# Optimization experiments

Hardware: AMD Instinct MI355X
Metric: run time of the kernel (lower is better)

Reference implementation:

```python
import jax, jax.numpy as jnp
import numpy as np

B = 8192          # batch
DIM = 2048        # feature dim
FANOUT = 10       # balanced 10-ary tree, depth 3 -> 1000 leaves
N_NODES = 1 + 10 + 100  # inner nodes with classifiers = 111
NUM_CLASSES = 1000


def setup_inputs() -> dict:
    key = jax.random.key(0)
    k1, k2, k3, k4 = jax.random.split(key, 4)
    x = jax.random.normal(k1, (B, DIM), dtype=jnp.float32)
    labels = jax.random.randint(k2, (B,), 0, NUM_CLASSES, dtype=jnp.int64 if jax.config.jax_enable_x64 else jnp.int32)
    # Stacked per-node Linear(dim, num_child+1): column 0 is the extra slot
    # included in the softmax but never routed to (children use cols 1..FANOUT).
    W = jax.random.normal(k3, (N_NODES, DIM, FANOUT + 1), dtype=jnp.float32) * (1.0 / np.sqrt(DIM))
    b = jax.random.normal(k4, (N_NODES, FANOUT + 1), dtype=jnp.float32) * 0.01
    return {"x": x, "labels": labels, "W": W, "b": b}


def reference(x, labels, W, b):
    # All 111 tiny per-node Linear+softmax classifiers fused into one batched GEMM.
    logits = jnp.einsum('bd,ndk->bnk', x, W) + b          # [B, 111, 11]
    probs = jax.nn.softmax(logits, axis=-1)               # softmax over num_child+1 (incl. dummy col 0)
    # Hierarchical path probabilities (root.path_prob = 1.0):
    # level-1 nodes are children of root (node 0), via softmax columns 1..10.
    p1 = probs[:, 0, 1:]                                   # [B, 10]
    # level-2 nodes: children of nodes 1..10
    p2 = (p1[:, :, None] * probs[:, 1:11, 1:]).reshape(x.shape[0], 100)    # [B, 100]
    # leaves: children of nodes 11..110 -> 1000 classes (out[:, 1:] slice already applied)
    out = (p2[:, :, None] * probs[:, 11:111, 1:]).reshape(x.shape[0], NUM_CLASSES)  # [B, 1000]
    penalty = jnp.float32(0.0)
    return (out, penalty)
```

## Files before the change

### kernel.cpp

```cpp
#include <hip/hip_runtime.h>
#include <hip/hip_bf16.h>
#include <hip/hip_fp16.h>

typedef _Float16 f16;
typedef __attribute__((ext_vector_type(8))) _Float16 f16x8;
typedef __attribute__((ext_vector_type(4))) float f32x4;

#define DIM     2048
#define BROWS   8192
#define NCOLS   1221
#define NPAD    1280
#define NNODES  111
#define BK      64
#define NKT     (DIM / BK)
#define IMG     8192
#define PANEL   (32 * IMG)

__global__ __launch_bounds__(256) void prep_x(const float* __restrict__ X,
                                              f16* __restrict__ Xf) {
    __shared__ float T[128 * 68];
    int blk = blockIdx.x;
    int mp = blk >> 5, kt = blk & 31;
    int t = threadIdx.x;
    int row = t >> 1, half = t & 1;
    const float* src = X + (size_t)(mp * 128 + row) * DIM + kt * 64 + half * 32;
    float* dst = T + row * 68 + half * 32;
    #pragma unroll
    for (int i = 0; i < 8; ++i) ((f32x4*)dst)[i] = ((const f32x4*)src)[i];
    __syncthreads();
    int w = t >> 6, l = t & 63, r = l & 15, q = l >> 4;
    f16* out = Xf + (size_t)blk * IMG;
    #pragma unroll
    for (int p = 0; p < 4; ++p) {
        int gk = p * 4 + w;
        int kk = gk >> 3, g = gk & 7;
        const float* s = T + (g * 16 + r) * 68 + kk * 32 + q * 8;
        f32x4 a = *(const f32x4*)s;
        f32x4 b = *(const f32x4*)(s + 4);
        f16x8 h;
        h[0] = (f16)a[0]; h[1] = (f16)a[1]; h[2] = (f16)a[2]; h[3] = (f16)a[3];
        h[4] = (f16)b[0]; h[5] = (f16)b[1]; h[6] = (f16)b[2]; h[7] = (f16)b[3];
        *(f16x8*)(out + (size_t)(p * 256 + t) * 8) = h;
    }
}

__global__ void prep_b(const float* __restrict__ W, f16* __restrict__ Bf) {
    int idx = blockIdx.x * 256 + threadIdx.x;
    int c = idx & 1023, img = idx >> 10;
    int np = img >> 5, kt = img & 31;
    int kk = c >> 9, g = (c >> 6) & 7, l = c & 63, r = l & 15, q = l >> 4;
    int col = np * 128 + g * 16 + r;
    int d0  = kt * 64 + kk * 32 + q * 8;
    f16x8 v;
    if (col < NCOLS) {
        int n = col / 11, k = col - n * 11;
        const float* src = W + ((size_t)n * DIM + d0) * 11 + k;
        #pragma unroll
        for (int e = 0; e < 8; ++e) v[e] = (f16)src[(size_t)e * 11];
    } else {
        #pragma unroll
        for (int e = 0; e < 8; ++e) v[e] = (f16)0.f;
    }
    *(f16x8*)(Bf + (size_t)idx * 8) = v;
}

__global__ __launch_bounds__(512, 2) void gemm_f16(const f16* __restrict__ Xf,
                                                   const f16* __restrict__ Bf,
                                                   f16* __restrict__ Lh) {
    __shared__ __align__(16) f16 As[2][16384];
    __shared__ __align__(16) f16 Bs[2][16384];

    int bid = blockIdx.x;
    int swz = (bid & 7) * 20 + (bid >> 3);
    int mt = swz / 5, nt = swz - mt * 5;

    int t = threadIdx.x, w = t >> 6, l = t & 63, r = l & 15, q = l >> 4;
    int wm = w >> 2, wn = w & 3;

    const f16* abase = Xf + (size_t)(mt * 2) * PANEL + (size_t)t * 8;
    const f16* bbase = Bf + (size_t)(nt * 2) * PANEL + (size_t)t * 8;

    f32x4 acc[8][4];
    #pragma unroll
    for (int i = 0; i < 8; ++i)
        #pragma unroll
        for (int j = 0; j < 4; ++j) acc[i][j] = (f32x4)0.f;

#define STAGE(KT, C)                                                              \
    {                                                                             \
        _Pragma("unroll")                                                         \
        for (int p = 0; p < 4; ++p) {                                             \
            __builtin_amdgcn_global_load_lds(                                     \
                (const __attribute__((address_space(1))) void*)                   \
                    (abase + (size_t)(p >> 1) * PANEL + (size_t)(KT) * IMG + (p & 1) * 4096), \
                (__attribute__((address_space(3))) void*)(&As[C][p * 4096 + w * 512]), 16, 0, 0); \
            __builtin_amdgcn_global_load_lds(                                     \
                (const __attribute__((address_space(1))) void*)                   \
                    (bbase + (size_t)(p >> 1) * PANEL + (size_t)(KT) * IMG + (p & 1) * 4096), \
                (__attribute__((address_space(3))) void*)(&Bs[C][p * 4096 + w * 512]), 16, 0, 0); \
        }                                                                         \
    }

#define COMPUTE(C)                                                                \
    {                                                                             \
        _Pragma("unroll")                                                         \
        for (int kk = 0; kk < 2; ++kk) {                                          \
            f16x8 af[8], bfr[4];                                                  \
            _Pragma("unroll")                                                     \
            for (int m = 0; m < 8; ++m)                                           \
                af[m] = *(const f16x8*)(&As[C][wm * 8192 + ((kk * 8 + m) * 64 + l) * 8]); \
            _Pragma("unroll")                                                     \
            for (int n = 0; n < 4; ++n)                                           \
                bfr[n] = *(const f16x8*)(&Bs[C][(wn >> 1) * 8192                  \
                            + ((kk * 8 + (wn & 1) * 4 + n) * 64 + l) * 8]);       \
            _Pragma("unroll")                                                     \
            for (int m = 0; m < 8; ++m)                                           \
                _Pragma("unroll")                                                 \
                for (int n = 0; n < 4; ++n)                                       \
                    acc[m][n] = __builtin_amdgcn_mfma_f32_16x16x32_f16(af[m], bfr[n], acc[m][n], 0, 0, 0); \
        }                                                                         \
    }

    STAGE(0, 0)

    for (int kt = 0; kt < NKT - 1; ++kt) {
        int cc = kt & 1, cn = cc ^ 1;
        STAGE(kt + 1, cn)
        asm volatile("s_waitcnt vmcnt(8)" ::: "memory");
        __builtin_amdgcn_s_barrier();
        COMPUTE(cc)
        asm volatile("s_waitcnt lgkmcnt(0)" ::: "memory");
        __builtin_amdgcn_s_barrier();
    }
    asm volatile("s_waitcnt vmcnt(0)" ::: "memory");
    __builtin_amdgcn_s_barrier();
    COMPUTE(1)

#undef STAGE
#undef COMPUTE

    #pragma unroll
    for (int m = 0; m < 8; ++m) {
        int row = mt * 256 + wm * 128 + m * 16 + q * 4;
        #pragma unroll
        for (int n = 0; n < 4; ++n) {
            int col = nt * 256 + wn * 64 + n * 16 + r;
            #pragma unroll
            for (int j = 0; j < 4; ++j)
                Lh[(size_t)(row + j) * NPAD + col] = (f16)acc[m][n][j];
        }
    }
}

__global__ void tree_epi(const f16* __restrict__ L, const float* __restrict__ bias,
                         float* __restrict__ out) {
    __shared__ float P[4][NNODES * 11];
    __shared__ f16 R[4][NPAD];
    int w = threadIdx.x >> 6, l = threadIdx.x & 63;
    int row = blockIdx.x * 4 + w;

    const f16x8* src = (const f16x8*)(L + (size_t)row * NPAD);
    f16x8* dst = (f16x8*)R[w];
    dst[l]      = src[l];
    dst[l + 64] = src[l + 64];
    if (l < 32) dst[l + 128] = src[l + 128];

    for (int n = l; n < NNODES; n += 64) {
        float v[11], mx = -1e30f;
        #pragma unroll
        for (int k = 0; k < 11; ++k) { v[k] = (float)R[w][n * 11 + k] + bias[n * 11 + k]; mx = fmaxf(mx, v[k]); }
        float s = 0.f;
        #pragma unroll
        for (int k = 0; k < 11; ++k) { v[k] = __expf(v[k] - mx); s += v[k]; }
        float inv = 1.f / s;
        #pragma unroll
        for (int k = 0; k < 11; ++k) P[w][n * 11 + k] = v[k] * inv;
    }
    __syncthreads();
    const float* Pw = P[w];
    for (int c = l; c < 1000; c += 64) {
        int i  = c / 100;
        int j  = (c % 100) / 10;
        int mm = c % 10;
        float p = Pw[1 + i] * Pw[(1 + i) * 11 + 1 + j] * Pw[(11 + 10 * i + j) * 11 + 1 + mm];
        out[(size_t)row * 1000 + c] = p;
    }
    if (row == 0 && threadIdx.x == 0) out[(size_t)BROWS * 1000] = 0.f;
}

extern "C" void kernel_launch(void* const* d_in, const int* in_sizes, int n_in,
                              void* d_out, int out_size, void* d_ws, size_t ws_size,
                              hipStream_t stream) {
    const float* x    = (const float*)d_in[0];
    const float* W    = (const float*)d_in[2];
    const float* bias = (const float*)d_in[3];
    float* out = (float*)d_out;

    f16* Xf = (f16*)d_ws;
    f16* Bf = (f16*)((char*)d_ws + 33554432);
    f16* Lh = (f16*)((char*)d_ws + 38797312);

    prep_x <<<64 * 32, 256, 0, stream>>>(x, Xf);
    prep_b <<<1280, 256, 0, stream>>>(W, Bf);
    gemm_f16<<<160, 512, 0, stream>>>(Xf, Bf, Lh);
    tree_epi<<<BROWS / 4, 256, 0, stream>>>(Lh, bias, out);
}
```

Before: 104.2 us.

## Interleave split-K loads with MFMA phases and merge prep kernels into one launch

The GEMM main loop now stages each half-K slice of the A and B tiles separately and interleaves those global-to-LDS loads with four smaller MFMA phases. Each phase is separated by barriers and surrounded by wave priority raising, with finer vmcnt waits. This is meant to overlap memory traffic with matrix math more evenly, at the cost of more barriers per iteration. The two prep kernels are also fused into one launch that branches on block index, saving one launch and letting X conversion and W conversion run concurrently.

```diff
diff --git a/kernel.cpp b/kernel.cpp
--- a/kernel.cpp
+++ b/kernel.cpp
@@ -12,56 +12,58 @@
 #define NPAD    1280
 #define NNODES  111
 #define BK      64
-#define NKT     (DIM / BK)
+#define NKT     32
 #define IMG     8192
 #define PANEL   (32 * IMG)
 
-__global__ __launch_bounds__(256) void prep_x(const float* __restrict__ X,
-                                              f16* __restrict__ Xf) {
+__global__ __launch_bounds__(256) void prep_all(const float* __restrict__ X,
+                                                const float* __restrict__ W,
+                                                f16* __restrict__ Xf,
+                                                f16* __restrict__ Bf) {
     __shared__ float T[128 * 68];
-    int blk = blockIdx.x;
-    int mp = blk >> 5, kt = blk & 31;
-    int t = threadIdx.x;
-    int row = t >> 1, half = t & 1;
-    const float* src = X + (size_t)(mp * 128 + row) * DIM + kt * 64 + half * 32;
-    float* dst = T + row * 68 + half * 32;
-    #pragma unroll
-    for (int i = 0; i < 8; ++i) ((f32x4*)dst)[i] = ((const f32x4*)src)[i];
-    __syncthreads();
-    int w = t >> 6, l = t & 63, r = l & 15, q = l >> 4;
-    f16* out = Xf + (size_t)blk * IMG;
-    #pragma unroll
-    for (int p = 0; p < 4; ++p) {
-        int gk = p * 4 + w;
-        int kk = gk >> 3, g = gk & 7;
-        const float* s = T + (g * 16 + r) * 68 + kk * 32 + q * 8;
-        f32x4 a = *(const f32x4*)s;
-        f32x4 b = *(const f32x4*)(s + 4);
-        f16x8 h;
-        h[0] = (f16)a[0]; h[1] = (f16)a[1]; h[2] = (f16)a[2]; h[3] = (f16)a[3];
-        h[4] = (f16)b[0]; h[5] = (f16)b[1]; h[6] = (f16)b[2]; h[7] = (f16)b[3];
-        *(f16x8*)(out + (size_t)(p * 256 + t) * 8) = h;
-    }
-}
-
-__global__ void prep_b(const float* __restrict__ W, f16* __restrict__ Bf) {
-    int idx = blockIdx.x * 256 + threadIdx.x;
-    int c = idx & 1023, img = idx >> 10;
-    int np = img >> 5, kt = img & 31;
-    int kk = c >> 9, g = (c >> 6) & 7, l = c & 63, r = l & 15, q = l >> 4;
-    int col = np * 128 + g * 16 + r;
-    int d0  = kt * 64 + kk * 32 + q * 8;
-    f16x8 v;
-    if (col < NCOLS) {
-        int n = col / 11, k = col - n * 11;
-        const float* src = W + ((size_t)n * DIM + d0) * 11 + k;
-        #pragma unroll
-        for (int e = 0; e < 8; ++e) v[e] = (f16)src[(size_t)e * 11];
+    int b = blockIdx.x;
+    if (b < 2048) {
+        int mp = b >> 5, kt = b & 31;
+        int t = threadIdx.x;
+        int row = t >> 1, half = t & 1;
+        const float* src = X + (size_t)(mp * 128 + row) * DIM + kt * 64 + half * 32;
+        float* dst = T + row * 68 + half * 32;
+        #pragma unroll
+        for (int i = 0; i < 8; ++i) ((f32x4*)dst)[i] = ((const f32x4*)src)[i];
+        __syncthreads();
+        int w = t >> 6, l = t & 63, r = l & 15, q = l >> 4;
+        f16* out = Xf + (size_t)b * IMG;
+        #pragma unroll
+        for (int p = 0; p < 4; ++p) {
+            int gk = p * 4 + w;
+            int kk = gk >> 3, g = gk & 7;
+            const float* s = T + (g * 16 + r) * 68 + kk * 32 + q * 8;
+            f32x4 a = *(const f32x4*)s;
+            f32x4 c = *(const f32x4*)(s + 4);
+            f16x8 h;
+            h[0] = (f16)a[0]; h[1] = (f16)a[1]; h[2] = (f16)a[2]; h[3] = (f16)a[3];
+            h[4] = (f16)c[0]; h[5] = (f16)c[1]; h[6] = (f16)c[2]; h[7] = (f16)c[3];
+            *(f16x8*)(out + (size_t)(p * 256 + t) * 8) = h;
+        }
     } else {
-        #pragma unroll
-        for (int e = 0; e < 8; ++e) v[e] = (f16)0.f;
-    }
-    *(f16x8*)(Bf + (size_t)idx * 8) = v;
+        int idx = (b - 2048) * 256 + threadIdx.x;
+        int c = idx & 1023, img = idx >> 10;
+        int np = img >> 5, kt = img & 31;
+        int kk = c >> 9, g = (c >> 6) & 7, l = c & 63, r = l & 15, q = l >> 4;
+        int col = np * 128 + g * 16 + r;
+        int d0  = kt * 64 + kk * 32 + q * 8;
+        f16x8 v;
+        if (col < NCOLS) {
+            int n = col / 11, k = col - n * 11;
+            const float* src = W + ((size_t)n * DIM + d0) * 11 + k;
+            #pragma unroll
+            for (int e = 0; e < 8; ++e) v[e] = (f16)src[(size_t)e * 11];
+        } else {
+            #pragma unroll
+            for (int e = 0; e < 8; ++e) v[e] = (f16)0.f;
+        }
+        *(f16x8*)(Bf + (size_t)idx * 8) = v;
+    }
 }
 
 __global__ __launch_bounds__(512, 2) void gemm_f16(const f16* __restrict__ Xf,
@@ -76,6 +78,7 @@
 
     int t = threadIdx.x, w = t >> 6, l = t & 63, r = l & 15, q = l >> 4;
     int wm = w >> 2, wn = w & 3;
+    int bpan = (wn >> 1) * 8192, bc4 = (wn & 1) * 4;
 
     const f16* abase = Xf + (size_t)(mt * 2) * PANEL + (size_t)t * 8;
     const f16* bbase = Bf + (size_t)(nt * 2) * PANEL + (size_t)t * 8;
@@ -86,58 +89,94 @@
         #pragma unroll
         for (int j = 0; j < 4; ++j) acc[i][j] = (f32x4)0.f;
 
-#define STAGE(KT, C)                                                              \
-    {                                                                             \
-        _Pragma("unroll")                                                         \
-        for (int p = 0; p < 4; ++p) {                                             \
-            __builtin_amdgcn_global_load_lds(                                     \
-                (const __attribute__((address_space(1))) void*)                   \
-                    (abase + (size_t)(p >> 1) * PANEL + (size_t)(KT) * IMG + (p & 1) * 4096), \
-                (__attribute__((address_space(3))) void*)(&As[C][p * 4096 + w * 512]), 16, 0, 0); \
-            __builtin_amdgcn_global_load_lds(                                     \
-                (const __attribute__((address_space(1))) void*)                   \
-                    (bbase + (size_t)(p >> 1) * PANEL + (size_t)(KT) * IMG + (p & 1) * 4096), \
-                (__attribute__((address_space(3))) void*)(&Bs[C][p * 4096 + w * 512]), 16, 0, 0); \
-        }                                                                         \
-    }
-
-#define COMPUTE(C)                                                                \
-    {                                                                             \
-        _Pragma("unroll")                                                         \
-        for (int kk = 0; kk < 2; ++kk) {                                          \
-            f16x8 af[8], bfr[4];                                                  \
-            _Pragma("unroll")                                                     \
-            for (int m = 0; m < 8; ++m)                                           \
-                af[m] = *(const f16x8*)(&As[C][wm * 8192 + ((kk * 8 + m) * 64 + l) * 8]); \
-            _Pragma("unroll")                                                     \
-            for (int n = 0; n < 4; ++n)                                           \
-                bfr[n] = *(const f16x8*)(&Bs[C][(wn >> 1) * 8192                  \
-                            + ((kk * 8 + (wn & 1) * 4 + n) * 64 + l) * 8]);       \
-            _Pragma("unroll")                                                     \
-            for (int m = 0; m < 8; ++m)                                           \
-                _Pragma("unroll")                                                 \
-                for (int n = 0; n < 4; ++n)                                       \
-                    acc[m][n] = __builtin_amdgcn_mfma_f32_16x16x32_f16(af[m], bfr[n], acc[m][n], 0, 0, 0); \
-        }                                                                         \
-    }
-
-    STAGE(0, 0)
-
-    for (int kt = 0; kt < NKT - 1; ++kt) {
-        int cc = kt & 1, cn = cc ^ 1;
-        STAGE(kt + 1, cn)
-        asm volatile("s_waitcnt vmcnt(8)" ::: "memory");
-        __builtin_amdgcn_s_barrier();
-        COMPUTE(cc)
-        asm volatile("s_waitcnt lgkmcnt(0)" ::: "memory");
-        __builtin_amdgcn_s_barrier();
-    }
-    asm volatile("s_waitcnt vmcnt(0)" ::: "memory");
-    __builtin_amdgcn_s_barrier();
-    COMPUTE(1)
-
-#undef STAGE
-#undef COMPUTE
+    f16x8 af[4], bfr[4];
+
+#define GLD(SRC, DST)                                                            \
+    __builtin_amdgcn_global_load_lds(                                            \
+        (const __attribute__((address_space(1))) void*)(SRC),                    \
+        (__attribute__((address_space(3))) void*)(DST), 16, 0, 0)
+#define STAGE_A(KT, C, KH)                                                       \
+    { GLD(abase + (size_t)(KT) * IMG + (KH) * 4096, &As[C][(KH) * 4096 + w * 512]);            \
+      GLD(abase + PANEL + (size_t)(KT) * IMG + (KH) * 4096, &As[C][(2 + (KH)) * 4096 + w * 512]); }
+#define STAGE_B(KT, C, KH)                                                       \
+    { GLD(bbase + (size_t)(KT) * IMG + (KH) * 4096, &Bs[C][(KH) * 4096 + w * 512]);            \
+      GLD(bbase + PANEL + (size_t)(KT) * IMG + (KH) * 4096, &Bs[C][(2 + (KH)) * 4096 + w * 512]); }
+#define DS_AF(C, KK, MH)                                                         \
+    { _Pragma("unroll")                                                          \
+      for (int m_ = 0; m_ < 4; ++m_)                                             \
+          af[m_] = *(const f16x8*)(&As[C][wm * 8192 + (((KK) * 8 + (MH) * 4 + m_) * 64 + l) * 8]); }
+#define DS_BF(C, KK)                                                             \
+    { _Pragma("unroll")                                                          \
+      for (int n_ = 0; n_ < 4; ++n_)                                             \
+          bfr[n_] = *(const f16x8*)(&Bs[C][bpan + (((KK) * 8 + bc4 + n_) * 64 + l) * 8]); }
+#define MFMA16(MH)                                                               \
+    { _Pragma("unroll")                                                          \
+      for (int m_ = 0; m_ < 4; ++m_)                                             \
+          _Pragma("unroll")                                                      \
+          for (int n_ = 0; n_ < 4; ++n_)                                         \
+              acc[(MH) * 4 + m_][n_] = __builtin_amdgcn_mfma_f32_16x16x32_f16(   \
+                  af[m_], bfr[n_], acc[(MH) * 4 + m_][n_], 0, 0, 0); }
+#define BAR __builtin_amdgcn_s_barrier()
+#define LGKM0 { asm volatile("s_waitcnt lgkmcnt(0)" ::: "memory");               \
+                __builtin_amdgcn_sched_barrier(0); }
+#define VM(N) asm volatile("s_waitcnt vmcnt(" #N ")" ::: "memory")
+#define PRIO1 __builtin_amdgcn_s_setprio(1)
+#define PRIO0 __builtin_amdgcn_s_setprio(0)
+
+#define ITER(KT, CC, CN)                                                         \
+    {                                                                    \
+      STAGE_A((KT) + 1, CN, 0)                                                   \
+      VM(6);                                                                     \
+      BAR;                                 \
+      DS_AF(CC, 0, 0) DS_BF(CC, 0)                                               \
+      LGKM0 PRIO1; MFMA16(0) PRIO0; BAR;                                         \
+                                                                         \
+      STAGE_B((KT) + 1, CN, 0)                                                   \
+      DS_AF(CC, 0, 1)                                                            \
+      LGKM0 PRIO1; MFMA16(1) PRIO0; BAR;                                         \
+                                                                         \
+      STAGE_A((KT) + 1, CN, 1)                                                   \
+      VM(6);                                                                     \
+      BAR;                                              \
+      DS_AF(CC, 1, 0) DS_BF(CC, 1)                                               \
+      LGKM0 PRIO1; MFMA16(0) PRIO0; BAR;                                         \
+                                                                         \
+      STAGE_B((KT) + 1, CN, 1)                                                   \
+      DS_AF(CC, 1, 1)                                                            \
+      LGKM0 PRIO1; MFMA16(1) PRIO0; BAR; }
+
+    STAGE_A(0, 0, 0) STAGE_B(0, 0, 0) STAGE_A(0, 0, 1) STAGE_B(0, 0, 1)
+
+    for (int kt = 0; kt < 30; kt += 2) {
+        ITER(kt,     0, 1)
+        ITER(kt + 1, 1, 0)
+    }
+    ITER(30, 0, 1)
+    VM(4);
+    BAR;
+    DS_AF(1, 0, 0) DS_BF(1, 0)
+    LGKM0 PRIO1; MFMA16(0) PRIO0;
+    DS_AF(1, 0, 1)
+    LGKM0 PRIO1; MFMA16(1) PRIO0;
+    VM(0);
+    BAR;
+    DS_AF(1, 1, 0) DS_BF(1, 1)
+    LGKM0 PRIO1; MFMA16(0) PRIO0;
+    DS_AF(1, 1, 1)
+    LGKM0 PRIO1; MFMA16(1) PRIO0;
+
+#undef GLD
+#undef STAGE_A
+#undef STAGE_B
+#undef DS_AF
+#undef DS_BF
+#undef MFMA16
+#undef BAR
+#undef LGKM0
+#undef VM
+#undef PRIO1
+#undef PRIO0
+#undef ITER
 
     #pragma unroll
     for (int m = 0; m < 8; ++m) {
@@ -200,8 +239,7 @@
     f16* Bf = (f16*)((char*)d_ws + 33554432);
     f16* Lh = (f16*)((char*)d_ws + 38797312);
 
-    prep_x <<<64 * 32, 256, 0, stream>>>(x, Xf);
-    prep_b <<<1280, 256, 0, stream>>>(W, Bf);
+    prep_all<<<2048 + 1280, 256, 0, stream>>>(x, W, Xf, Bf);
     gemm_f16<<<160, 512, 0, stream>>>(Xf, Bf, Lh);
     tree_epi<<<BROWS / 4, 256, 0, stream>>>(Lh, bias, out);
 }
```

Result: faster. 96.05 us (-7.8%).
